# Kernel optimization log

Hardware: AMD Instinct MI355X
Metric: run time of the kernel (lower is better)

## Reference

```python
import jax, jax.numpy as jnp
import numpy as np

B = 65536
NUM_NODES = 6
EMB = 128      # node_embedding_dim
HID = 256      # graph_hidden_dim
LAT = 64       # latent_dim
PROJ = 512     # graph_projection_dim
VOCAB = 46     # num_lotto_numbers + 1
NEG_SLOPE = 0.2
MASK_VAL = -1e9


def setup_inputs() -> dict:
    key = jax.random.key(0)
    ks = jax.random.split(key, 16)
    numbers = jax.random.randint(ks[0], (B, NUM_NODES), 0, VOCAB, dtype=jnp.int64 if jax.config.jax_enable_x64 else jnp.int32)
    adj = jax.random.uniform(ks[1], (B, NUM_NODES, NUM_NODES), dtype=jnp.float32)
    s = lambda k, shape, fan_in: jax.random.normal(k, shape, jnp.float32) / np.sqrt(fan_in)
    return {
        "numbers": numbers,
        "adj": adj,
        "emb": s(ks[2], (VOCAB, EMB), EMB),
        "W0": s(ks[3], (EMB, HID), EMB),
        "a0": s(ks[4], (2 * HID, 1), 2 * HID),
        "W1": s(ks[5], (HID, HID), HID),
        "a1": s(ks[6], (2 * HID, 1), 2 * HID),
        "W2": s(ks[7], (HID, HID), HID),
        "a2": s(ks[8], (2 * HID, 1), 2 * HID),
        "P1_w": s(ks[9], (NUM_NODES * HID, PROJ), NUM_NODES * HID),
        "P1_b": jnp.zeros((PROJ,), jnp.float32),
        "P2_w": s(ks[10], (PROJ, 2 * LAT), PROJ),
        "P2_b": jnp.zeros((2 * LAT,), jnp.float32),
    }


def _gat_layer(h, adj, W, a):
    # h: [B, N, F_in], adj: [B, N, N], W: [F_in, F_out], a: [2*F_out, 1]
    Wh = jnp.einsum("bnf,fo->bno", h, W)                      # [B, N, F_out]
    # a([Wh_i || Wh_j]) == Wh_i @ a_src + Wh_j @ a_dst (avoids [B,N,N,2F] tensor)
    F_out = W.shape[1]
    a_src = Wh @ a[:F_out, 0]                                  # [B, N]
    a_dst = Wh @ a[F_out:, 0]                                  # [B, N]
    e = jax.nn.leaky_relu(a_src[:, :, None] + a_dst[:, None, :], NEG_SLOPE)
    e = jnp.where(adj == 0, MASK_VAL, e)
    attention = jax.nn.softmax(e, axis=-1)                     # dropout = identity (eval)
    return jnp.einsum("bij,bjo->bio", attention, Wh)           # [B, N, F_out]


def reference(numbers, adj, emb, W0, a0, W1, a1, W2, a2, P1_w, P1_b, P2_w, P2_b):
    h = emb[numbers]                                           # [B, 6, EMB]
    for W, a in ((W0, a0), (W1, a1), (W2, a2)):
        h = jax.nn.relu(_gat_layer(h, adj, W, a))
    graph_repr = h.reshape(h.shape[0], -1)                     # [B, 6*HID]
    x = jax.nn.relu(graph_repr @ P1_w + P1_b)                  # [B, PROJ]
    latent_params = x @ P2_w + P2_b                            # [B, 2*LAT]
    mu, logvar = jnp.split(latent_params, 2, axis=-1)
    return (mu, logvar)
```

## Files before the change

kernel.cpp:

```cpp
#include <hip/hip_runtime.h>
#include <math.h>

#define BTOT  65536
#define NN    6
#define NEG   0.2f
#define MASKV (-1e9f)

typedef short bf16x8 __attribute__((ext_vector_type(8)));
typedef float f32x4  __attribute__((ext_vector_type(4)));

#define OFF_W0 0u
#define OFF_W1 131072u
#define OFF_W2 393216u
#define OFF_P1 655360u
#define OFF_P2 3801088u
#define WS_NEED 4063232ull

__device__ __forceinline__ f32x4 mfma16(bf16x8 a, bf16x8 b, f32x4 c){
  return __builtin_amdgcn_mfma_f32_16x16x32_bf16(a, b, c, 0, 0, 0);
}

#define BAR() do { \
  asm volatile("s_waitcnt lgkmcnt(0)" ::: "memory"); \
  __builtin_amdgcn_s_barrier(); \
  asm volatile("" ::: "memory"); \
} while (0)

#define WH_BASE 24576

__device__ __forceinline__ int hwordL(int r, int c){
  return WH_BASE + r*264 + (c ^ ((r&7)<<2));
}

__device__ __forceinline__ int ACH(int frag, int p, int kk){
  return (frag*64 + (p ^ (kk&7) ^ ((p>>4)&3)))*8;
}

__device__ __forceinline__ void split4(float4 x, ushort4& h, ushort4& l){
  float xs[4] = {x.x, x.y, x.z, x.w};
  unsigned hu[4], lu[4];
  #pragma unroll
  for (int e=0;e<4;++e){
    unsigned u = __float_as_uint(xs[e]);
    float hf = __uint_as_float(u & 0xFFFF0000u);
    hu[e] = u >> 16;
    lu[e] = __float_as_uint(xs[e] - hf) >> 16;
  }
  h = make_ushort4((unsigned short)hu[0],(unsigned short)hu[1],
                   (unsigned short)hu[2],(unsigned short)hu[3]);
  l = make_ushort4((unsigned short)lu[0],(unsigned short)lu[1],
                   (unsigned short)lu[2],(unsigned short)lu[3]);
}

__global__ __launch_bounds__(64) void fragize(
    const float* __restrict__ W0, const float* __restrict__ W1,
    const float* __restrict__ W2, const float* __restrict__ P1w,
    const float* __restrict__ P2w, char* __restrict__ ws)
{
  int fid = blockIdx.x;
  int lane = threadIdx.x;
  const float* src; int KK, N; unsigned off; int idx;
  if (fid < 64)        { src = W0;  KK = 4;  N = 256; off = OFF_W0; idx = fid; }
  else if (fid < 192)  { src = W1;  KK = 8;  N = 256; off = OFF_W1; idx = fid - 64; }
  else if (fid < 320)  { src = W2;  KK = 8;  N = 256; off = OFF_W2; idx = fid - 192; }
  else if (fid < 1856) { src = P1w; KK = 48; N = 512; off = OFF_P1; idx = fid - 320; }
  else                 { src = P2w; KK = 16; N = 128; off = OFF_P2; idx = fid - 1856; }
  int nt = idx / KK, kk = idx % KK;
  int n  = nt*16 + (lane & 15);
  int kb = kk*32 + (lane >> 4)*8;
  bf16x8 h, l;
  #pragma unroll
  for (int e=0;e<8;++e){
    float x = src[(size_t)(kb+e)*N + n];
    unsigned u = __float_as_uint(x);
    float hf = __uint_as_float(u & 0xFFFF0000u);
    h[e] = (short)(u >> 16);
    l[e] = (short)(__float_as_uint(x - hf) >> 16);
  }
  char* dst = ws + off + (size_t)idx*2048 + (size_t)lane*16;
  *(bf16x8*)dst = h;
  *(bf16x8*)(dst + 1024) = l;
}

#define GLOADSET(S, kv) do{ \
    (S)[0] = *(const bf16x8*)(wb0 + (kv)*2048); \
    (S)[1] = *(const bf16x8*)(wb0 + (kv)*2048 + 1024); \
    (S)[2] = *(const bf16x8*)(wb1 + (kv)*2048); \
    (S)[3] = *(const bf16x8*)(wb1 + (kv)*2048 + 1024); } while(0)

template<int KK>
__device__ __forceinline__ void do_gemm(const unsigned short* ab,
    const char* __restrict__ wf, int g, int wl, int lane, f32x4 (&acc)[3][2])
{
  const int nq = wl;
  #pragma unroll
  for (int mt=0;mt<3;++mt){
    acc[mt][0] = f32x4{0.f,0.f,0.f,0.f};
    acc[mt][1] = f32x4{0.f,0.f,0.f,0.f};
  }
  const char* wb0 = wf + (size_t)(2*nq)*KK*2048 + (size_t)lane*16;
  const char* wb1 = wb0 + (size_t)KK*2048;
  bf16x8 B[3][4];
  GLOADSET(B[0], 0);
  GLOADSET(B[1], 1);
  const int abase = g*48;
  #pragma unroll
  for (int kk=0; kk<KK; ++kk){
    if (kk+2 < KK) GLOADSET(B[(kk+2)%3], kk+2);
    if (kk == KK/2) BAR();
    #pragma unroll
    for (int mt=0; mt<3; ++mt){
      bf16x8 ah = *(const bf16x8*)(ab + ACH(abase + mt*KK + kk,          lane, kk));
      bf16x8 al = *(const bf16x8*)(ab + ACH(abase + 3*KK + mt*KK + kk,   lane, kk));
      acc[mt][0] = mfma16(ah, B[kk%3][0], acc[mt][0]);
      acc[mt][1] = mfma16(ah, B[kk%3][2], acc[mt][1]);
      acc[mt][0] = mfma16(al, B[kk%3][0], acc[mt][0]);
      acc[mt][1] = mfma16(al, B[kk%3][2], acc[mt][1]);
      acc[mt][0] = mfma16(ah, B[kk%3][1], acc[mt][0]);
      acc[mt][1] = mfma16(ah, B[kk%3][3], acc[mt][1]);
    }
  }
  BAR();
}

__device__ __forceinline__ void write_gr(unsigned short* ab, const float (*nh)[4],
    const float* rsum, int item_blk, int lane)
{
  const int kkl  = lane >> 3;
  const int kg2  = (lane >> 1) & 3;
  const int elem = (lane & 1) * 4;
  #pragma unroll
  for (int i=0;i<NN;++i){
    float rinv = 1.0f / rsum[i];
    float4 v;
    v.x = fmaxf(nh[i][0]*rinv, 0.f);
    v.y = fmaxf(nh[i][1]*rinv, 0.f);
    v.z = fmaxf(nh[i][2]*rinv, 0.f);
    v.w = fmaxf(nh[i][3]*rinv, 0.f);
    ushort4 hv, lv; split4(v, hv, lv);
    int kkg = i*8 + kkl;
    int p   = kg2*16 + item_blk;
    *(ushort4*)(ab + ACH(kkg,      p, kkg) + elem) = hv;
    *(ushort4*)(ab + ACH(48 + kkg, p, kkg) + elem) = lv;
  }
}

template<int MODE>
__device__ __forceinline__ void do_whattn(float* hb, unsigned short* ab,
    const f32x4 (&acc)[3][2], const float* __restrict__ avec,
    int g, int wl, int lane, unsigned long long mz,
    float (*nhold)[4], float* rshold)
{
  const int arow = lane & 15, kgrp = lane >> 4;
  const int nq = wl;
  #pragma unroll
  for (int mt=0;mt<3;++mt)
    #pragma unroll
    for (int nt=0;nt<2;++nt)
      #pragma unroll
      for (int v=0;v<4;++v)
        hb[hwordL(mt*16 + kgrp*4 + v, (nq*2+nt)*16 + arow)] = acc[mt][nt][v];
  BAR();

  const int c0 = lane << 2;
  float wh[NN][4];
  #pragma unroll
  for (int i=0;i<NN;++i){
    float4 t = *(const float4*)(hb + hwordL(wl*NN+i, c0));
    wh[i][0]=t.x; wh[i][1]=t.y; wh[i][2]=t.z; wh[i][3]=t.w;
  }
  float4 as4 = *(const float4*)(avec + c0);
  float4 ad4 = *(const float4*)(avec + 256 + c0);
  float ps[NN], pd[NN];
  #pragma unroll
  for (int i=0;i<NN;++i){
    ps[i] = wh[i][0]*as4.x + wh[i][1]*as4.y + wh[i][2]*as4.z + wh[i][3]*as4.w;
    pd[i] = wh[i][0]*ad4.x + wh[i][1]*ad4.y + wh[i][2]*ad4.z + wh[i][3]*ad4.w;
  }
  for (int off=32; off>0; off>>=1){
    #pragma unroll
    for (int i=0;i<NN;++i){ ps[i]+=__shfl_xor(ps[i],off); pd[i]+=__shfl_xor(pd[i],off); }
  }
  float rmax[NN];
  #pragma unroll
  for (int i=0;i<NN;++i) rmax[i] = -3.4e38f;
  #pragma unroll
  for (int i=0;i<NN;++i){
    #pragma unroll
    for (int j=0;j<NN;++j){
      float e = ps[i] + pd[j];
      e = (e > 0.f) ? e : NEG*e;
      if ((mz >> (i*6+j)) & 1ull) e = MASKV;
      rmax[i] = fmaxf(rmax[i], e);
    }
  }
  float rsum[NN] = {0.f,0.f,0.f,0.f,0.f,0.f};
  float nh[NN][4];
  #pragma unroll
  for (int i=0;i<NN;++i){ nh[i][0]=0.f; nh[i][1]=0.f; nh[i][2]=0.f; nh[i][3]=0.f; }
  #pragma unroll
  for (int j=0;j<NN;++j){
    float s[NN];
    #pragma unroll
    for (int i=0;i<NN;++i){
      float e = ps[i] + pd[j];
      e = (e > 0.f) ? e : NEG*e;
      if ((mz >> (i*6+j)) & 1ull) e = MASKV;
      s[i] = __expf(e - rmax[i]);
      rsum[i] += s[i];
    }
    #pragma unroll
    for (int i=0;i<NN;++i){
      nh[i][0] = fmaf(s[i], wh[j][0], nh[i][0]);
      nh[i][1] = fmaf(s[i], wh[j][1], nh[i][1]);
      nh[i][2] = fmaf(s[i], wh[j][2], nh[i][2]);
      nh[i][3] = fmaf(s[i], wh[j][3], nh[i][3]);
    }
  }

  if (MODE == 0){
    const int kkl  = lane >> 3;
    const int kg2  = (lane >> 1) & 3;
    const int elem = (lane & 1) * 4;
    #pragma unroll
    for (int i=0;i<NN;++i){
      float rinv = 1.0f / rsum[i];
      float4 v;
      v.x = fmaxf(nh[i][0]*rinv, 0.f);
      v.y = fmaxf(nh[i][1]*rinv, 0.f);
      v.z = fmaxf(nh[i][2]*rinv, 0.f);
      v.w = fmaxf(nh[i][3]*rinv, 0.f);
      ushort4 hv, lv; split4(v, hv, lv);
      int rl = wl*NN + i;
      int mt = rl >> 4;
      int p  = kg2*16 + (rl & 15);
      *(ushort4*)(ab + ACH(g*48 + mt*8 + kkl,      p, kkl) + elem) = hv;
      *(ushort4*)(ab + ACH(g*48 + 24 + mt*8 + kkl, p, kkl) + elem) = lv;
    }
  } else if (MODE == 1){
    #pragma unroll
    for (int i=0;i<NN;++i){
      nhold[i][0]=nh[i][0]; nhold[i][1]=nh[i][1];
      nhold[i][2]=nh[i][2]; nhold[i][3]=nh[i][3];
      rshold[i]=rsum[i];
    }
  } else {
    write_gr(ab, nh, rsum, g*8 + wl, lane);
  }
  BAR();
}

__device__ __forceinline__ void idle_step(){ BAR(); BAR(); }

__global__ __launch_bounds__(1024) void nge_mfma(
    const int* __restrict__ numbers, const float* __restrict__ adj,
    const float* __restrict__ emb,
    const float* __restrict__ a0, const float* __restrict__ a1,
    const float* __restrict__ a2,
    const float* __restrict__ P1b, const float* __restrict__ P2b,
    const char* __restrict__ wfrag, float* __restrict__ out)
{
  __shared__ float hb[37248];
  unsigned short* ab = (unsigned short*)hb;

  const int tid  = threadIdx.x;
  const int lane = tid & 63;
  const int w    = tid >> 6;
  const int g    = w >> 3;
  const int wl   = w & 7;
  const int itemg = blockIdx.x*16 + w;

  {
    int rows[NN];
    #pragma unroll
    for (int i=0;i<NN;++i) rows[i] = numbers[itemg*NN + i];
    const int half = lane >> 5;
    const int c0   = (lane & 31) << 2;
    const int kk4  = c0 >> 5;
    const int kg2  = (c0 >> 3) & 3;
    const int elem = c0 & 7;
    #pragma unroll
    for (int base=0; base<3; ++base){
      int i = base*2 + half;
      float4 v = *(const float4*)(emb + (size_t)rows[i]*128 + c0);
      ushort4 hv, lv; split4(v, hv, lv);
      int rl = wl*NN + i;
      int mt = rl >> 4;
      int p  = kg2*16 + (rl & 15);
      *(ushort4*)(ab + ACH(g*48 + mt*4 + kk4,      p, kk4) + elem) = hv;
      *(ushort4*)(ab + ACH(g*48 + 12 + mt*4 + kk4, p, kk4) + elem) = lv;
    }
  }
  unsigned long long mz;
  {
    float av = (lane < 36) ? adj[(size_t)itemg*36 + lane] : 1.0f;
    mz = __ballot((lane < 36) && (av == 0.0f));
  }
  BAR();

  f32x4 acc[3][2];
  float nhold[NN][4]; float rshold[NN];

  if (g == 0) do_gemm<4>(ab, wfrag + OFF_W0, 0, wl, lane, acc);
  else        idle_step();
  if (g == 0) do_whattn<0>(hb, ab, acc, a0, 0, wl, lane, mz, nhold, rshold);
  else        do_gemm<4>(ab, wfrag + OFF_W0, 1, wl, lane, acc);
  if (g == 0) do_gemm<8>(ab, wfrag + OFF_W1, 0, wl, lane, acc);
  else        do_whattn<0>(hb, ab, acc, a0, 1, wl, lane, mz, nhold, rshold);
  if (g == 0) do_whattn<0>(hb, ab, acc, a1, 0, wl, lane, mz, nhold, rshold);
  else        do_gemm<8>(ab, wfrag + OFF_W1, 1, wl, lane, acc);
  if (g == 0) do_gemm<8>(ab, wfrag + OFF_W2, 0, wl, lane, acc);
  else        do_whattn<0>(hb, ab, acc, a1, 1, wl, lane, mz, nhold, rshold);
  if (g == 0) do_whattn<1>(hb, ab, acc, a2, 0, wl, lane, mz, nhold, rshold);
  else        do_gemm<8>(ab, wfrag + OFF_W2, 1, wl, lane, acc);
  if (g == 0){ write_gr(ab, nhold, rshold, wl, lane); BAR(); BAR(); }
  else        do_whattn<2>(hb, ab, acc, a2, 1, wl, lane, mz, nhold, rshold);

  const int arow = lane & 15, kgrp = lane >> 4;

  {
    f32x4 pa[2][2];
    pa[0][0]=f32x4{0.f,0.f,0.f,0.f}; pa[0][1]=f32x4{0.f,0.f,0.f,0.f};
    pa[1][0]=f32x4{0.f,0.f,0.f,0.f}; pa[1][1]=f32x4{0.f,0.f,0.f,0.f};
    const char* wb0 = wfrag + OFF_P1 + (size_t)(2*w)*48*2048 + (size_t)lane*16;
    const char* wb1 = wb0 + (size_t)48*2048;
    bf16x8 B[4][4];
    GLOADSET(B[0], 0);
    GLOADSET(B[1], 1);
    GLOADSET(B[2], 2);
    #pragma unroll
    for (int kk=0; kk<48; ++kk){
      if (kk+3 < 48) GLOADSET(B[(kk+3)%4], kk+3);
      const int par = kk & 1;
      bf16x8 ah = *(const bf16x8*)(ab + ACH(kk,      lane, kk));
      bf16x8 al = *(const bf16x8*)(ab + ACH(48 + kk, lane, kk));
      pa[par][0] = mfma16(ah, B[kk%4][0], pa[par][0]);
      pa[par][1] = mfma16(ah, B[kk%4][2], pa[par][1]);
      pa[par][0] = mfma16(al, B[kk%4][0], pa[par][0]);
      pa[par][1] = mfma16(al, B[kk%4][2], pa[par][1]);
      pa[par][0] = mfma16(ah, B[kk%4][1], pa[par][0]);
      pa[par][1] = mfma16(ah, B[kk%4][3], pa[par][1]);
    }
    f32x4 pa0, pa1;
    #pragma unroll
    for (int v=0;v<4;++v){ pa0[v] = pa[0][0][v] + pa[1][0][v];
                           pa1[v] = pa[0][1][v] + pa[1][1][v]; }
    BAR();
    #pragma unroll
    for (int nt=0;nt<2;++nt){
      int col = (2*w+nt)*16 + arow;
      float bv = P1b[col];
      f32x4 pv = nt ? pa1 : pa0;
      int kkx   = w;
      int kgrpx = nt*2 + (arow >> 3);
      int elem  = arow & 7;
      #pragma unroll
      for (int v=0;v<4;++v){
        int item = kgrp*4 + v;
        int p = kgrpx*16 + item;
        float val = fmaxf(pv[v] + bv, 0.f);
        unsigned u = __float_as_uint(val);
        float hf = __uint_as_float(u & 0xFFFF0000u);
        ab[ACH(kkx,      p, kkx) + elem] = (unsigned short)(u >> 16);
        ab[ACH(16 + kkx, p, kkx) + elem] = (unsigned short)(__float_as_uint(val - hf) >> 16);
      }
    }
    BAR();
  }

  {
    float* scr = hb + 8192;
    const int colt  = w & 7;
    const int khalf = w >> 3;
    f32x4 pc = {0.f,0.f,0.f,0.f};
    const char* qb = wfrag + OFF_P2 + (size_t)colt*16*2048 + (size_t)lane*16;
    bf16x8 C[3][2];
    #define QLOADSET(S, kv) do{ \
      (S)[0] = *(const bf16x8*)(qb + (kv)*2048); \
      (S)[1] = *(const bf16x8*)(qb + (kv)*2048 + 1024); } while(0)
    QLOADSET(C[0], khalf*8 + 0);
    QLOADSET(C[1], khalf*8 + 1);
    #pragma unroll
    for (int j=0; j<8; ++j){
      int kk = khalf*8 + j;
      if (j+2 < 8) QLOADSET(C[(j+2)%3], kk+2);
      bf16x8 ah = *(const bf16x8*)(ab + ACH(kk,      lane, kk));
      bf16x8 al = *(const bf16x8*)(ab + ACH(16 + kk, lane, kk));
      pc = mfma16(ah, C[j%3][0], pc);
      pc = mfma16(al, C[j%3][0], pc);
      pc = mfma16(ah, C[j%3][1], pc);
    }
    if (khalf == 1)
      *(f32x4*)(scr + colt*256 + lane*4) = pc;
    BAR();
    if (khalf == 0){
      f32x4 other = *(const f32x4*)(scr + colt*256 + lane*4);
      int col = colt*16 + arow;
      float bv = P2b[col];
      #pragma unroll
      for (int v=0;v<4;++v){
        int itl = kgrp*4 + v;
        size_t ig = (size_t)blockIdx.x*16 + itl;
        float val = pc[v] + other[v] + bv;
        if (col < 64) out[ig*64 + col] = val;
        else          out[(size_t)BTOT*64 + ig*64 + (col - 64)] = val;
      }
    }
  }
}

#define EMBD  128
#define HIDD  256
#define PROJD 512
#define LAT2  128
#define TI    16
#define NTHR  1024

template<int K, bool LAST>
__device__ __forceinline__ void gat_layer(
    float* hb, float* st,
    const float* __restrict__ W,
    const float* __restrict__ avec,
    int item, int lane, int tid,
    unsigned long long mz)
{
    const int c0 = lane << 2;
    float wh[NN][4];
    #pragma unroll
    for (int i = 0; i < NN; ++i)
        #pragma unroll
        for (int c = 0; c < 4; ++c) wh[i][c] = 0.f;
    const float* hitem = hb + item * (NN * HIDD);
    for (int k0 = 0; k0 < K; k0 += 32) {
        __syncthreads();
        {
            const int cc = (tid & 63) << 2;
            const int r0 = tid >> 6;
            *(float4*)(st + r0 * HIDD + cc) =
                *(const float4*)(W + (size_t)(k0 + r0) * HIDD + cc);
            *(float4*)(st + (r0 + 16) * HIDD + cc) =
                *(const float4*)(W + (size_t)(k0 + r0 + 16) * HIDD + cc);
        }
        __syncthreads();
        #pragma unroll
        for (int k = 0; k < 32; ++k) {
            const float* hr = hitem + (k0 + k) * NN;
            float2 h01 = *(const float2*)(hr + 0);
            float2 h23 = *(const float2*)(hr + 2);
            float2 h45 = *(const float2*)(hr + 4);
            float av[NN] = {h01.x, h01.y, h23.x, h23.y, h45.x, h45.y};
            float4 bv = *(const float4*)(st + k * HIDD + c0);
            #pragma unroll
            for (int i = 0; i < NN; ++i) {
                wh[i][0] = fmaf(av[i], bv.x, wh[i][0]);
                wh[i][1] = fmaf(av[i], bv.y, wh[i][1]);
                wh[i][2] = fmaf(av[i], bv.z, wh[i][2]);
                wh[i][3] = fmaf(av[i], bv.w, wh[i][3]);
            }
        }
    }
    float4 as4 = *(const float4*)(avec + c0);
    float4 ad4 = *(const float4*)(avec + HIDD + c0);
    float ps[NN], pd[NN];
    #pragma unroll
    for (int i = 0; i < NN; ++i) {
        ps[i] = wh[i][0]*as4.x + wh[i][1]*as4.y + wh[i][2]*as4.z + wh[i][3]*as4.w;
        pd[i] = wh[i][0]*ad4.x + wh[i][1]*ad4.y + wh[i][2]*ad4.z + wh[i][3]*ad4.w;
    }
    for (int off = 32; off > 0; off >>= 1) {
        #pragma unroll
        for (int i = 0; i < NN; ++i) {
            ps[i] += __shfl_xor(ps[i], off);
            pd[i] += __shfl_xor(pd[i], off);
        }
    }
    float rmax[NN];
    #pragma unroll
    for (int i = 0; i < NN; ++i) rmax[i] = -3.4e38f;
    #pragma unroll
    for (int i = 0; i < NN; ++i) {
        #pragma unroll
        for (int j = 0; j < NN; ++j) {
            float e = ps[i] + pd[j];
            e = (e > 0.f) ? e : NEG * e;
            if ((mz >> (i * 6 + j)) & 1ull) e = MASKV;
            rmax[i] = fmaxf(rmax[i], e);
        }
    }
    float rsum[NN] = {0.f, 0.f, 0.f, 0.f, 0.f, 0.f};
    float nh[NN][4];
    #pragma unroll
    for (int i = 0; i < NN; ++i)
        #pragma unroll
        for (int c = 0; c < 4; ++c) nh[i][c] = 0.f;
    #pragma unroll
    for (int j = 0; j < NN; ++j) {
        float s[NN];
        #pragma unroll
        for (int i = 0; i < NN; ++i) {
            float e = ps[i] + pd[j];
            e = (e > 0.f) ? e : NEG * e;
            if ((mz >> (i * 6 + j)) & 1ull) e = MASKV;
            s[i] = expf(e - rmax[i]);
            rsum[i] += s[i];
        }
        #pragma unroll
        for (int i = 0; i < NN; ++i) {
            nh[i][0] = fmaf(s[i], wh[j][0], nh[i][0]);
            nh[i][1] = fmaf(s[i], wh[j][1], nh[i][1]);
            nh[i][2] = fmaf(s[i], wh[j][2], nh[i][2]);
            nh[i][3] = fmaf(s[i], wh[j][3], nh[i][3]);
        }
    }
    float* hout = hb + item * (NN * HIDD);
    #pragma unroll
    for (int i = 0; i < NN; ++i) {
        float rinv = 1.0f / rsum[i];
        if (LAST) {
            float4 v;
            v.x = fmaxf(nh[i][0] * rinv, 0.f);
            v.y = fmaxf(nh[i][1] * rinv, 0.f);
            v.z = fmaxf(nh[i][2] * rinv, 0.f);
            v.w = fmaxf(nh[i][3] * rinv, 0.f);
            *(float4*)(hout + i * HIDD + c0) = v;
        } else {
            #pragma unroll
            for (int c = 0; c < 4; ++c)
                hout[(c0 + c) * NN + i] = fmaxf(nh[i][c] * rinv, 0.f);
        }
    }
}

__global__ __launch_bounds__(NTHR) void nge_fused(
    const int* __restrict__ numbers,
    const float* __restrict__ adj,
    const float* __restrict__ emb,
    const float* __restrict__ W0, const float* __restrict__ a0,
    const float* __restrict__ W1, const float* __restrict__ a1,
    const float* __restrict__ W2, const float* __restrict__ a2,
    const float* __restrict__ P1w, const float* __restrict__ P1b,
    const float* __restrict__ P2w, const float* __restrict__ P2b,
    float* __restrict__ out)
{
    __shared__ float hbuf[TI * NN * HIDD];
    __shared__ float stage[12288];
    const int tid  = threadIdx.x;
    const int lane = tid & 63;
    const int item = tid >> 6;
    const int bidx = blockIdx.x * TI + item;
    {
        int rows[NN];
        #pragma unroll
        for (int i = 0; i < NN; ++i) rows[i] = numbers[bidx * NN + i];
        float* hitem = hbuf + item * (NN * HIDD);
        #pragma unroll
        for (int i = 0; i < NN; ++i) {
            #pragma unroll
            for (int r = 0; r < 2; ++r) {
                int f = lane + (r << 6);
                hitem[f * NN + i] = emb[rows[i] * EMBD + f];
            }
        }
    }
    unsigned long long mz;
    {
        float av = (lane < 36) ? adj[(size_t)bidx * 36 + lane] : 1.0f;
        mz = __ballot((lane < 36) && (av == 0.0f));
    }
    gat_layer<EMBD, false>(hbuf, stage, W0, a0, item, lane, tid, mz);
    gat_layer<HIDD, false>(hbuf, stage, W1, a1, item, lane, tid, mz);
    gat_layer<HIDD, true >(hbuf, stage, W2, a2, item, lane, tid, mz);
    const int ct  = tid & 127;
    const int rt  = tid >> 7;
    const int pc0 = ct << 2;
    float acc[2][4];
    #pragma unroll
    for (int t = 0; t < 2; ++t)
        #pragma unroll
        for (int c = 0; c < 4; ++c) acc[t][c] = 0.f;
    for (int g0 = 0; g0 < NN * HIDD; g0 += 24) {
        __syncthreads();
        #pragma unroll
        for (int s = 0; s < 3; ++s) {
            int r = rt + 8 * s;
            *(float4*)(stage + r * PROJD + pc0) =
                *(const float4*)(P1w + (size_t)(g0 + r) * PROJD + pc0);
        }
        __syncthreads();
        #pragma unroll
        for (int r4 = 0; r4 < 24; r4 += 4) {
            float4 A0 = *(const float4*)(hbuf + rt * (NN * HIDD) + g0 + r4);
            float4 A1 = *(const float4*)(hbuf + (rt + 8) * (NN * HIDD) + g0 + r4);
            const float a0v[4] = {A0.x, A0.y, A0.z, A0.w};
            const float a1v[4] = {A1.x, A1.y, A1.z, A1.w};
            #pragma unroll
            for (int rr = 0; rr < 4; ++rr) {
                float4 bv = *(const float4*)(stage + (r4 + rr) * PROJD + pc0);
                acc[0][0] = fmaf(a0v[rr], bv.x, acc[0][0]);
                acc[0][1] = fmaf(a0v[rr], bv.y, acc[0][1]);
                acc[0][2] = fmaf(a0v[rr], bv.z, acc[0][2]);
                acc[0][3] = fmaf(a0v[rr], bv.w, acc[0][3]);
                acc[1][0] = fmaf(a1v[rr], bv.x, acc[1][0]);
                acc[1][1] = fmaf(a1v[rr], bv.y, acc[1][1]);
                acc[1][2] = fmaf(a1v[rr], bv.z, acc[1][2]);
                acc[1][3] = fmaf(a1v[rr], bv.w, acc[1][3]);
            }
        }
    }
    __syncthreads();
    {
        float4 b1 = *(const float4*)(P1b + pc0);
        #pragma unroll
        for (int t = 0; t < 2; ++t) {
            int it = rt + 8 * t;
            float4 xv;
            xv.x = fmaxf(acc[t][0] + b1.x, 0.f);
            xv.y = fmaxf(acc[t][1] + b1.y, 0.f);
            xv.z = fmaxf(acc[t][2] + b1.z, 0.f);
            xv.w = fmaxf(acc[t][3] + b1.w, 0.f);
            *(float4*)(hbuf + it * PROJD + pc0) = xv;
        }
    }
    const int j0 = lane << 1;
    float acc2x = 0.f, acc2y = 0.f;
    for (int g0 = 0; g0 < PROJD; g0 += 64) {
        __syncthreads();
        {
            int r  = tid >> 5;
            int cc = (tid & 31) << 2;
            *(float4*)(stage + r * LAT2 + cc) =
                *(const float4*)(P2w + (size_t)(g0 + r) * LAT2 + cc);
            *(float4*)(stage + (r + 32) * LAT2 + cc) =
                *(const float4*)(P2w + (size_t)(g0 + r + 32) * LAT2 + cc);
        }
        __syncthreads();
        const float* xit = hbuf + item * PROJD + g0;
        #pragma unroll
        for (int r4 = 0; r4 < 64; r4 += 4) {
            float4 A = *(const float4*)(xit + r4);
            const float av[4] = {A.x, A.y, A.z, A.w};
            #pragma unroll
            for (int rr = 0; rr < 4; ++rr) {
                float2 bv = *(const float2*)(stage + (r4 + rr) * LAT2 + j0);
                acc2x = fmaf(av[rr], bv.x, acc2x);
                acc2y = fmaf(av[rr], bv.y, acc2y);
            }
        }
    }
    {
        float o0 = acc2x + P2b[j0];
        float o1 = acc2y + P2b[j0 + 1];
        size_t base = (size_t)bidx * 64;
        float2 v; v.x = o0; v.y = o1;
        if (j0 < 64) {
            *(float2*)(out + base + j0) = v;
        } else {
            *(float2*)(out + (size_t)BTOT * 64 + base + (j0 - 64)) = v;
        }
    }
}

extern "C" void kernel_launch(void* const* d_in, const int* in_sizes, int n_in,
                              void* d_out, int out_size, void* d_ws, size_t ws_size,
                              hipStream_t stream) {
    const int*   numbers = (const int*)  d_in[0];
    const float* adj     = (const float*)d_in[1];
    const float* emb     = (const float*)d_in[2];
    const float* W0      = (const float*)d_in[3];
    const float* a0      = (const float*)d_in[4];
    const float* W1      = (const float*)d_in[5];
    const float* a1      = (const float*)d_in[6];
    const float* W2      = (const float*)d_in[7];
    const float* a2      = (const float*)d_in[8];
    const float* P1w     = (const float*)d_in[9];
    const float* P1b     = (const float*)d_in[10];
    const float* P2w     = (const float*)d_in[11];
    const float* P2b     = (const float*)d_in[12];
    float* out = (float*)d_out;

    if (ws_size >= WS_NEED) {
        char* ws = (char*)d_ws;
        fragize<<<1984, 64, 0, stream>>>(W0, W1, W2, P1w, P2w, ws);
        nge_mfma<<<BTOT/16, 1024, 0, stream>>>(numbers, adj, emb,
                                               a0, a1, a2, P1b, P2b, ws, out);
    } else {
        nge_fused<<<BTOT/TI, NTHR, 0, stream>>>(numbers, adj, emb,
                                                W0, a0, W1, a1, W2, a2,
                                                P1w, P1b, P2w, P2b, out);
    }
}
```

Baseline: 1.184 ms.

## Fold attention vectors into weights as extra MFMA column to compute scores

Precomputes W·a_src and W·a_dst per GAT layer in the prep kernel and stores them as a bf16-split MFMA fragment. During each layer GEMM, otherwise idle waves (wl>=5) multiply the input rows by this fragment to produce the attention logits directly, which go to a small LDS buffer. This removes the per-wave dot product and 6-step shuffle reduction in the attention phase. It also adds s_setprio around MFMA blocks and simplifies the row-max computation using monotonicity of leaky ReLU. The logits now come from h·(Wa) in split-bf16 rather than from (hW)·a in fp32, which slightly changes rounding. The fast path also requires a larger workspace.

```diff
diff --git a/kernel.cpp b/kernel.cpp
--- a/kernel.cpp
+++ b/kernel.cpp
@@ -15,6 +15,10 @@
 #define OFF_P1 655360u
 #define OFF_P2 3801088u
 #define WS_NEED 4063232ull
+#define OFF_AS0 4063232u
+#define OFF_AS1 4071424u
+#define OFF_AS2 4087808u
+#define WS_NEED_AS 4104192ull
 
 __device__ __forceinline__ f32x4 mfma16(bf16x8 a, bf16x8 b, f32x4 c){
   return __builtin_amdgcn_mfma_f32_16x16x32_bf16(a, b, c, 0, 0, 0);
@@ -31,7 +35,6 @@
 __device__ __forceinline__ int hwordL(int r, int c){
   return WH_BASE + r*264 + (c ^ ((r&7)<<2));
 }
-
 __device__ __forceinline__ int ACH(int frag, int p, int kk){
   return (frag*64 + (p ^ (kk&7) ^ ((p>>4)&3)))*8;
 }
@@ -55,10 +58,45 @@
 __global__ __launch_bounds__(64) void fragize(
     const float* __restrict__ W0, const float* __restrict__ W1,
     const float* __restrict__ W2, const float* __restrict__ P1w,
-    const float* __restrict__ P2w, char* __restrict__ ws)
+    const float* __restrict__ P2w,
+    const float* __restrict__ a0v, const float* __restrict__ a1v,
+    const float* __restrict__ a2v, char* __restrict__ ws)
 {
   int fid = blockIdx.x;
   int lane = threadIdx.x;
+  if (fid >= 1984){
+    int idx = fid - 1984;
+    const float* W; const float* av; unsigned off; int kk;
+    if (idx < 4)       { W = W0; av = a0v; off = OFF_AS0; kk = idx; }
+    else if (idx < 12) { W = W1; av = a1v; off = OFF_AS1; kk = idx - 4; }
+    else               { W = W2; av = a2v; off = OFF_AS2; kk = idx - 12; }
+    int col = lane & 15;
+    int kb  = kk*32 + (lane >> 4)*8;
+    bf16x8 h, l;
+    #pragma unroll
+    for (int e=0;e<8;++e){
+      float x = 0.f;
+      if (col < 2){
+        const float* ap = av + col*256;
+        const float* wrow = W + (size_t)(kb+e)*256;
+        float acc = 0.f;
+        for (int o=0;o<256;o+=4){
+          float4 wv = *(const float4*)(wrow + o);
+          float4 a4 = *(const float4*)(ap + o);
+          acc += wv.x*a4.x + wv.y*a4.y + wv.z*a4.z + wv.w*a4.w;
+        }
+        x = acc;
+      }
+      unsigned u = __float_as_uint(x);
+      float hf = __uint_as_float(u & 0xFFFF0000u);
+      h[e] = (short)(u >> 16);
+      l[e] = (short)(__float_as_uint(x - hf) >> 16);
+    }
+    char* dst = ws + off + (size_t)kk*2048 + (size_t)lane*16;
+    *(bf16x8*)dst = h;
+    *(bf16x8*)(dst + 1024) = l;
+    return;
+  }
   const float* src; int KK, N; unsigned off; int idx;
   if (fid < 64)        { src = W0;  KK = 4;  N = 256; off = OFF_W0; idx = fid; }
   else if (fid < 192)  { src = W1;  KK = 8;  N = 256; off = OFF_W1; idx = fid - 64; }
@@ -88,37 +126,68 @@
     (S)[2] = *(const bf16x8*)(wb1 + (kv)*2048); \
     (S)[3] = *(const bf16x8*)(wb1 + (kv)*2048 + 1024); } while(0)
 
-template<int KK>
+template<int KK, bool AS>
 __device__ __forceinline__ void do_gemm(const unsigned short* ab,
-    const char* __restrict__ wf, int g, int wl, int lane, f32x4 (&acc)[3][2])
+    const char* __restrict__ wf, const char* __restrict__ wfS,
+    int g, int wl, int lane, f32x4 (&acc)[3][2], float* psd)
 {
-  const int nq = wl;
   #pragma unroll
   for (int mt=0;mt<3;++mt){
     acc[mt][0] = f32x4{0.f,0.f,0.f,0.f};
     acc[mt][1] = f32x4{0.f,0.f,0.f,0.f};
   }
-  const char* wb0 = wf + (size_t)(2*nq)*KK*2048 + (size_t)lane*16;
+  const char* wb0 = wf + (size_t)(2*wl)*KK*2048 + (size_t)lane*16;
   const char* wb1 = wb0 + (size_t)KK*2048;
   bf16x8 B[3][4];
   GLOADSET(B[0], 0);
   GLOADSET(B[1], 1);
+  const bool doX = AS && (wl >= 5);
+  const int mtx = wl - 5;
+  const char* wbS = wfS + (size_t)lane*16;
+  bf16x8 S[3][2];
+  f32x4 accX = {0.f,0.f,0.f,0.f};
+  if (doX){
+    S[0][0] = *(const bf16x8*)(wbS);
+    S[0][1] = *(const bf16x8*)(wbS + 1024);
+    S[1][0] = *(const bf16x8*)(wbS + 2048);
+    S[1][1] = *(const bf16x8*)(wbS + 2048 + 1024);
+  }
   const int abase = g*48;
   #pragma unroll
   for (int kk=0; kk<KK; ++kk){
-    if (kk+2 < KK) GLOADSET(B[(kk+2)%3], kk+2);
+    if (kk+2 < KK){
+      GLOADSET(B[(kk+2)%3], kk+2);
+      if (doX){
+        S[(kk+2)%3][0] = *(const bf16x8*)(wbS + (kk+2)*2048);
+        S[(kk+2)%3][1] = *(const bf16x8*)(wbS + (kk+2)*2048 + 1024);
+      }
+    }
     if (kk == KK/2) BAR();
     #pragma unroll
     for (int mt=0; mt<3; ++mt){
-      bf16x8 ah = *(const bf16x8*)(ab + ACH(abase + mt*KK + kk,          lane, kk));
-      bf16x8 al = *(const bf16x8*)(ab + ACH(abase + 3*KK + mt*KK + kk,   lane, kk));
+      bf16x8 ah = *(const bf16x8*)(ab + ACH(abase + mt*KK + kk,        lane, kk));
+      bf16x8 al = *(const bf16x8*)(ab + ACH(abase + 3*KK + mt*KK + kk, lane, kk));
+      __builtin_amdgcn_s_setprio(1);
       acc[mt][0] = mfma16(ah, B[kk%3][0], acc[mt][0]);
       acc[mt][1] = mfma16(ah, B[kk%3][2], acc[mt][1]);
       acc[mt][0] = mfma16(al, B[kk%3][0], acc[mt][0]);
       acc[mt][1] = mfma16(al, B[kk%3][2], acc[mt][1]);
       acc[mt][0] = mfma16(ah, B[kk%3][1], acc[mt][0]);
       acc[mt][1] = mfma16(ah, B[kk%3][3], acc[mt][1]);
-    }
+      if (doX && mt == mtx){
+        accX = mfma16(ah, S[kk%3][0], accX);
+        accX = mfma16(al, S[kk%3][0], accX);
+        accX = mfma16(ah, S[kk%3][1], accX);
+      }
+      __builtin_amdgcn_s_setprio(0);
+    }
+  }
+  if (doX && (lane & 15) < 2){
+    int colx  = lane & 15;
+    int rbase = mtx*16 + (lane >> 4)*4;
+    #pragma unroll
+    for (int v=0;v<4;++v)
+      psd[g*96 + (rbase+v)*2 + colx] = accX[v];
   }
   BAR();
 }
@@ -145,21 +214,20 @@
   }
 }
 
-template<int MODE>
+template<int MODE, bool AS>
 __device__ __forceinline__ void do_whattn(float* hb, unsigned short* ab,
     const f32x4 (&acc)[3][2], const float* __restrict__ avec,
     int g, int wl, int lane, unsigned long long mz,
-    float (*nhold)[4], float* rshold)
+    float (*nhold)[4], float* rshold, const float* psd)
 {
   const int arow = lane & 15, kgrp = lane >> 4;
-  const int nq = wl;
   #pragma unroll
   for (int mt=0;mt<3;++mt)
     #pragma unroll
     for (int nt=0;nt<2;++nt)
       #pragma unroll
       for (int v=0;v<4;++v)
-        hb[hwordL(mt*16 + kgrp*4 + v, (nq*2+nt)*16 + arow)] = acc[mt][nt][v];
+        hb[hwordL(mt*16 + kgrp*4 + v, (wl*2+nt)*16 + arow)] = acc[mt][nt][v];
   BAR();
 
   const int c0 = lane << 2;
@@ -169,30 +237,38 @@
     float4 t = *(const float4*)(hb + hwordL(wl*NN+i, c0));
     wh[i][0]=t.x; wh[i][1]=t.y; wh[i][2]=t.z; wh[i][3]=t.w;
   }
-  float4 as4 = *(const float4*)(avec + c0);
-  float4 ad4 = *(const float4*)(avec + 256 + c0);
   float ps[NN], pd[NN];
+  if (AS){
+    #pragma unroll
+    for (int i=0;i<NN;++i){
+      float2 t = *(const float2*)(psd + g*96 + (wl*NN+i)*2);
+      ps[i] = t.x; pd[i] = t.y;
+    }
+  } else {
+    float4 as4 = *(const float4*)(avec + c0);
+    float4 ad4 = *(const float4*)(avec + 256 + c0);
+    #pragma unroll
+    for (int i=0;i<NN;++i){
+      ps[i] = wh[i][0]*as4.x + wh[i][1]*as4.y + wh[i][2]*as4.z + wh[i][3]*as4.w;
+      pd[i] = wh[i][0]*ad4.x + wh[i][1]*ad4.y + wh[i][2]*ad4.z + wh[i][3]*ad4.w;
+    }
+    for (int off=32; off>0; off>>=1){
+      #pragma unroll
+      for (int i=0;i<NN;++i){ ps[i]+=__shfl_xor(ps[i],off); pd[i]+=__shfl_xor(pd[i],off); }
+    }
+  }
+  float rmax[NN];
   #pragma unroll
   for (int i=0;i<NN;++i){
-    ps[i] = wh[i][0]*as4.x + wh[i][1]*as4.y + wh[i][2]*as4.z + wh[i][3]*as4.w;
-    pd[i] = wh[i][0]*ad4.x + wh[i][1]*ad4.y + wh[i][2]*ad4.z + wh[i][3]*ad4.w;
-  }
-  for (int off=32; off>0; off>>=1){
-    #pragma unroll
-    for (int i=0;i<NN;++i){ ps[i]+=__shfl_xor(ps[i],off); pd[i]+=__shfl_xor(pd[i],off); }
-  }
-  float rmax[NN];
-  #pragma unroll
-  for (int i=0;i<NN;++i) rmax[i] = -3.4e38f;
-  #pragma unroll
-  for (int i=0;i<NN;++i){
+    float mp = -3.4e38f;
     #pragma unroll
     for (int j=0;j<NN;++j){
-      float e = ps[i] + pd[j];
-      e = (e > 0.f) ? e : NEG*e;
-      if ((mz >> (i*6+j)) & 1ull) e = MASKV;
-      rmax[i] = fmaxf(rmax[i], e);
-    }
+      float pj = ((mz >> (i*6+j)) & 1ull) ? -3.4e38f : pd[j];
+      mp = fmaxf(mp, pj);
+    }
+    float t  = ps[i] + mp;
+    float lk = fmaxf(t, NEG*t);
+    rmax[i] = fmaxf(lk, MASKV);
   }
   float rsum[NN] = {0.f,0.f,0.f,0.f,0.f,0.f};
   float nh[NN][4];
@@ -203,9 +279,9 @@
     float s[NN];
     #pragma unroll
     for (int i=0;i<NN;++i){
-      float e = ps[i] + pd[j];
-      e = (e > 0.f) ? e : NEG*e;
-      if ((mz >> (i*6+j)) & 1ull) e = MASKV;
+      float t = ps[i] + pd[j];
+      float e = fmaxf(t, NEG*t);
+      e = ((mz >> (i*6+j)) & 1ull) ? MASKV : e;
       s[i] = __expf(e - rmax[i]);
       rsum[i] += s[i];
     }
@@ -252,6 +328,7 @@
 
 __device__ __forceinline__ void idle_step(){ BAR(); BAR(); }
 
+template<bool AS>
 __global__ __launch_bounds__(1024) void nge_mfma(
     const int* __restrict__ numbers, const float* __restrict__ adj,
     const float* __restrict__ emb,
@@ -260,8 +337,9 @@
     const float* __restrict__ P1b, const float* __restrict__ P2b,
     const char* __restrict__ wfrag, float* __restrict__ out)
 {
-  __shared__ float hb[37248];
+  __shared__ float hb[37440];
   unsigned short* ab = (unsigned short*)hb;
+  float* psd = hb + 37248;
 
   const int tid  = threadIdx.x;
   const int lane = tid & 63;
@@ -301,20 +379,27 @@
   f32x4 acc[3][2];
   float nhold[NN][4]; float rshold[NN];
 
-  if (g == 0) do_gemm<4>(ab, wfrag + OFF_W0, 0, wl, lane, acc);
+  const char* AS0 = wfrag + OFF_AS0;
+  const char* AS1 = wfrag + OFF_AS1;
+  const char* AS2 = wfrag + OFF_AS2;
+
+  if (g == 0) do_gemm<4,AS>(ab, wfrag + OFF_W0, AS0, 0, wl, lane, acc, psd);
   else        idle_step();
-  if (g == 0) do_whattn<0>(hb, ab, acc, a0, 0, wl, lane, mz, nhold, rshold);
-  else        do_gemm<4>(ab, wfrag + OFF_W0, 1, wl, lane, acc);
-  if (g == 0) do_gemm<8>(ab, wfrag + OFF_W1, 0, wl, lane, acc);
-  else        do_whattn<0>(hb, ab, acc, a0, 1, wl, lane, mz, nhold, rshold);
-  if (g == 0) do_whattn<0>(hb, ab, acc, a1, 0, wl, lane, mz, nhold, rshold);
-  else        do_gemm<8>(ab, wfrag + OFF_W1, 1, wl, lane, acc);
-  if (g == 0) do_gemm<8>(ab, wfrag + OFF_W2, 0, wl, lane, acc);
-  else        do_whattn<0>(hb, ab, acc, a1, 1, wl, lane, mz, nhold, rshold);
-  if (g == 0) do_whattn<1>(hb, ab, acc, a2, 0, wl, lane, mz, nhold, rshold);
-  else        do_gemm<8>(ab, wfrag + OFF_W2, 1, wl, lane, acc);
+  if (g == 0) do_whattn<0,AS>(hb, ab, acc, a0, 0, wl, lane, mz, nhold, rshold, psd);
+  else        do_gemm<4,AS>(ab, wfrag + OFF_W0, AS0, 1, wl, lane, acc, psd);
+
+  if (g == 0) do_gemm<8,AS>(ab, wfrag + OFF_W1, AS1, 0, wl, lane, acc, psd);
+  else        do_whattn<0,AS>(hb, ab, acc, a0, 1, wl, lane, mz, nhold, rshold, psd);
+  if (g == 0) do_whattn<0,AS>(hb, ab, acc, a1, 0, wl, lane, mz, nhold, rshold, psd);
+  else        do_gemm<8,AS>(ab, wfrag + OFF_W1, AS1, 1, wl, lane, acc, psd);
+
+  if (g == 0) do_gemm<8,AS>(ab, wfrag + OFF_W2, AS2, 0, wl, lane, acc, psd);
+  else        do_whattn<0,AS>(hb, ab, acc, a1, 1, wl, lane, mz, nhold, rshold, psd);
+  if (g == 0) do_whattn<1,AS>(hb, ab, acc, a2, 0, wl, lane, mz, nhold, rshold, psd);
+  else        do_gemm<8,AS>(ab, wfrag + OFF_W2, AS2, 1, wl, lane, acc, psd);
+
   if (g == 0){ write_gr(ab, nhold, rshold, wl, lane); BAR(); BAR(); }
-  else        do_whattn<2>(hb, ab, acc, a2, 1, wl, lane, mz, nhold, rshold);
+  else        do_whattn<2,AS>(hb, ab, acc, a2, 1, wl, lane, mz, nhold, rshold, psd);
 
   const int arow = lane & 15, kgrp = lane >> 4;
 
@@ -334,12 +419,14 @@
       const int par = kk & 1;
       bf16x8 ah = *(const bf16x8*)(ab + ACH(kk,      lane, kk));
       bf16x8 al = *(const bf16x8*)(ab + ACH(48 + kk, lane, kk));
+      __builtin_amdgcn_s_setprio(1);
       pa[par][0] = mfma16(ah, B[kk%4][0], pa[par][0]);
       pa[par][1] = mfma16(ah, B[kk%4][2], pa[par][1]);
       pa[par][0] = mfma16(al, B[kk%4][0], pa[par][0]);
       pa[par][1] = mfma16(al, B[kk%4][2], pa[par][1]);
       pa[par][0] = mfma16(ah, B[kk%4][1], pa[par][0]);
       pa[par][1] = mfma16(ah, B[kk%4][3], pa[par][1]);
+      __builtin_amdgcn_s_setprio(0);
     }
     f32x4 pa0, pa1;
     #pragma unroll
@@ -386,9 +473,11 @@
       if (j+2 < 8) QLOADSET(C[(j+2)%3], kk+2);
       bf16x8 ah = *(const bf16x8*)(ab + ACH(kk,      lane, kk));
       bf16x8 al = *(const bf16x8*)(ab + ACH(16 + kk, lane, kk));
+      __builtin_amdgcn_s_setprio(1);
       pc = mfma16(ah, C[j%3][0], pc);
       pc = mfma16(al, C[j%3][0], pc);
       pc = mfma16(ah, C[j%3][1], pc);
+      __builtin_amdgcn_s_setprio(0);
     }
     if (khalf == 1)
       *(f32x4*)(scr + colt*256 + lane*4) = pc;
@@ -678,11 +767,16 @@
     const float* P2b     = (const float*)d_in[12];
     float* out = (float*)d_out;
 
-    if (ws_size >= WS_NEED) {
+    if (ws_size >= WS_NEED_AS) {
         char* ws = (char*)d_ws;
-        fragize<<<1984, 64, 0, stream>>>(W0, W1, W2, P1w, P2w, ws);
-        nge_mfma<<<BTOT/16, 1024, 0, stream>>>(numbers, adj, emb,
-                                               a0, a1, a2, P1b, P2b, ws, out);
+        fragize<<<2004, 64, 0, stream>>>(W0, W1, W2, P1w, P2w, a0, a1, a2, ws);
+        nge_mfma<true><<<BTOT/16, 1024, 0, stream>>>(numbers, adj, emb,
+                                                     a0, a1, a2, P1b, P2b, ws, out);
+    } else if (ws_size >= WS_NEED) {
+        char* ws = (char*)d_ws;
+        fragize<<<1984, 64, 0, stream>>>(W0, W1, W2, P1w, P2w, a0, a1, a2, ws);
+        nge_mfma<false><<<BTOT/16, 1024, 0, stream>>>(numbers, adj, emb,
+                                                      a0, a1, a2, P1b, P2b, ws, out);
     } else {
         nge_fused<<<BTOT/TI, NTHR, 0, stream>>>(numbers, adj, emb,
                                                 W0, a0, W1, a1, W2, a2,
```

Result: faster. 1.084 ms (-8.5%).
